# Kernel tuning notes

Measured on AMD Instinct MI355X. Metric: run time of the kernel, lower is better.

The kernel has to match this reference:

```python
import jax, jax.numpy as jnp
import numpy as np
import math

B, Q, CQ = 2, 2048, 512
H, D = 8, 64  # no_heads, c_hidden

def setup_inputs() -> dict:
    key = jax.random.key(0)
    ks = jax.random.split(key, 8)
    s = 0.02
    return {
        "q_x": jax.random.normal(ks[0], (B, Q, CQ), jnp.float32),
        "kv_x": jax.random.normal(ks[1], (B, Q, CQ), jnp.float32),
        "bias": jax.random.normal(ks[2], (B, 1, Q, Q), jnp.float32),
        "w_qkv": jax.random.normal(ks[3], (3 * H * D, CQ), jnp.float32) * s,
        "w_o": jax.random.normal(ks[4], (CQ, H * D), jnp.float32) * s,
        "b_o": jnp.zeros((CQ,), jnp.float32),
        "w_g": jax.random.normal(ks[5], (H * D, CQ), jnp.float32) * s,
        "b_g": jnp.zeros((H * D,), jnp.float32),
    }

def reference(q_x, kv_x, bias, w_qkv, w_o, b_o, w_g, b_g):
    # Fused QKV projection from q_x (kv_x is unused by the original module's _prep_qkv)
    qkv = jnp.einsum('bqc,ec->bqe', q_x, w_qkv)  # [B,Q,3*H*D]
    q, k, v = jnp.split(qkv, 3, axis=-1)
    q = q.reshape(B, Q, H, D) / math.sqrt(D)
    k = k.reshape(B, Q, H, D)
    v = v.reshape(B, Q, H, D)
    # scores + additive pairwise bias, softmax over keys
    scores = jnp.einsum('bqhd,bkhd->bhqk', q, k) + bias  # [B,H,Q,K]
    attn = jax.nn.softmax(scores, axis=-1)
    o = jnp.einsum('bhqk,bkhd->bqhd', attn, v)  # [B,Q,H,D]
    # sigmoid gating
    g = jax.nn.sigmoid(jnp.einsum('bqc,ec->bqe', q_x, w_g) + b_g).reshape(B, Q, H, D)
    o = o * g
    # output projection
    o = o.reshape(B, Q, H * D)
    return jnp.einsum('bqe,ce->bqc', o, w_o) + b_o
```

## Files before the change

kernel.cpp:

```cpp
#include <hip/hip_runtime.h>
#include <math.h>

#define B_  2
#define Q_  2048
#define CQ_ 512
#define H_  8
#define D_  64
#define M_  (B_*Q_)
#define L2E 1.44269504088896f

typedef __bf16 bf16;
typedef __bf16 bf16x4 __attribute__((ext_vector_type(4)));
typedef __bf16 bf16x8 __attribute__((ext_vector_type(8)));
typedef float  f32x4  __attribute__((ext_vector_type(4)));
typedef float  f32x16 __attribute__((ext_vector_type(16)));

__device__ __forceinline__ void gl_lds16(const bf16* g, bf16* l) {
    __builtin_amdgcn_global_load_lds(
        (const __attribute__((address_space(1))) unsigned int*)g,
        (__attribute__((address_space(3))) unsigned int*)l, 16, 0, 0);
}

__device__ __forceinline__ bf16x4 shfl_xor32(bf16x4 v) {
    union { bf16x4 h; int i[2]; } u;
    u.h = v;
    u.i[0] = __shfl_xor(u.i[0], 32, 64);
    u.i[1] = __shfl_xor(u.i[1], 32, 64);
    return u.h;
}

#define S0 (4096*512)
#define S1 (1536*512)
#define S2 (512*512)
#define S3 (512*512)
__global__ __launch_bounds__(256)
void convert_kernel(const float* __restrict__ qx, const float* __restrict__ wqkv,
                    const float* __restrict__ wg, const float* __restrict__ wo,
                    bf16* __restrict__ qxb, bf16* __restrict__ wcat, bf16* __restrict__ wob)
{
    const long long t = (long long)blockIdx.x * 256 + threadIdx.x;
    const long long e = t * 8;
    const float* src; bf16* dst;
    if (e < S0) {
        const int m = (int)(e >> 9), k = (int)(e & 511);
        src = qx + e;
        dst = qxb + (size_t)(k >> 5) * (4096 * 32) + (size_t)m * 32 + (k & 31);
    } else if (e < S0 + S1) {
        const long long e2 = e - S0;
        const int n = (int)(e2 >> 9), k = (int)(e2 & 511);
        src = wqkv + e2;
        dst = wcat + (size_t)(k >> 5) * (2048 * 32) + (size_t)n * 32 + (k & 31);
    } else if (e < S0 + S1 + S2) {
        const long long e2 = e - S0 - S1;
        const int n = 1536 + (int)(e2 >> 9), k = (int)(e2 & 511);
        src = wg + e2;
        dst = wcat + (size_t)(k >> 5) * (2048 * 32) + (size_t)n * 32 + (k & 31);
    } else {
        const long long e2 = e - S0 - S1 - S2;
        const int n = (int)(e2 >> 9), k = (int)(e2 & 511);
        src = wo + e2;
        dst = wob + (size_t)(k >> 5) * (512 * 32) + (size_t)n * 32 + (k & 31);
    }
    const float4 a = *(const float4*)(src);
    const float4 b = *(const float4*)(src + 4);
    bf16x8 v;
    v[0] = (bf16)a.x; v[1] = (bf16)a.y; v[2] = (bf16)a.z; v[3] = (bf16)a.w;
    v[4] = (bf16)b.x; v[5] = (bf16)b.y; v[6] = (bf16)b.z; v[7] = (bf16)b.w;
    *(bf16x8*)dst = v;
}

template<int BM, int BN, int EPI, int WNR, int APACK>
__global__ __launch_bounds__(256)
void gemm_bf16(const bf16* __restrict__ A, const bf16* __restrict__ W,
               const float* __restrict__ bvec, float* __restrict__ fout,
               bf16* __restrict__ qb, bf16* __restrict__ kb, bf16* __restrict__ vb,
               bf16* __restrict__ gb)
{
    constexpr int MI = BM / 32, NJ = BN / 32;
    constexpr int APARTS = BM / 16, BPARTS = BN / 16, NPARTS = APARTS + BPARTS;
    __shared__ __align__(16) bf16 As[2][BM * 32];
    __shared__ __align__(16) bf16 Bs[2][BN * 32];

    const int t = threadIdx.x;
    const int w = t >> 6, lane = t & 63;
    const int l15 = lane & 15, quad = lane >> 4;
    const int wm = w & 1, wn = w >> 1;
    const int bm = blockIdx.x * BM;
    const int bn = blockIdx.y * BN;
    const bool swapped = (EPI == 1) || ((bn >> 9) != 2);

    f32x4 acc[MI][NJ] = {};

    auto stage = [&](int kp, int buf) {
        #pragma unroll
        for (int idx = 0; idx < NPARTS / 4; ++idx) {
            const int p = idx * 4 + w;
            if (p < APARTS) {
                if constexpr (APACK)
                    gl_lds16(A + (size_t)kp * (4096 * 32) + (size_t)bm * 32 + p * 512 + lane * 8,
                             As[buf] + p * 512);
                else
                    gl_lds16(A + (size_t)(bm + p * 16 + (lane >> 2)) * 512 + kp * 32 + (lane & 3) * 8,
                             As[buf] + p * 512);
            } else {
                gl_lds16(W + (size_t)kp * (WNR * 32) + (size_t)bn * 32 + (p - APARTS) * 512 + lane * 8,
                         Bs[buf] + (p - APARTS) * 512);
            }
        }
    };

    stage(0, 0);
    __asm__ volatile("s_waitcnt vmcnt(0)" ::: "memory");
    __syncthreads();

    int cur = 0;
    #pragma unroll 1
    for (int kp = 0; kp < 16; ++kp) {
        if (kp < 15) stage(kp + 1, cur ^ 1);

        bf16x8 af[MI], bfr[NJ];
        #pragma unroll
        for (int i = 0; i < MI; ++i)
            af[i] = *(const bf16x8*)(As[cur] + (wm * (BM / 2) + i * 16 + l15) * 32 + quad * 8);
        #pragma unroll
        for (int j = 0; j < NJ; ++j)
            bfr[j] = *(const bf16x8*)(Bs[cur] + (wn * (BN / 2) + j * 16 + l15) * 32 + quad * 8);
        if (swapped) {
            #pragma unroll
            for (int i = 0; i < MI; ++i)
                #pragma unroll
                for (int j = 0; j < NJ; ++j)
                    acc[i][j] = __builtin_amdgcn_mfma_f32_16x16x32_bf16(bfr[j], af[i], acc[i][j], 0, 0, 0);
        } else {
            #pragma unroll
            for (int i = 0; i < MI; ++i)
                #pragma unroll
                for (int j = 0; j < NJ; ++j)
                    acc[i][j] = __builtin_amdgcn_mfma_f32_16x16x32_bf16(af[i], bfr[j], acc[i][j], 0, 0, 0);
        }
        __asm__ volatile("s_waitcnt vmcnt(0)" ::: "memory");
        __syncthreads();
        cur ^= 1;
    }

    if (swapped) {
        #pragma unroll
        for (int i = 0; i < MI; ++i) {
            const int m = bm + wm * (BM / 2) + i * 16 + l15;
            const int b = m >> 11, qq = m & 2047;
            #pragma unroll
            for (int j = 0; j < NJ; ++j) {
                const int n0 = bn + wn * (BN / 2) + j * 16 + quad * 4;
                const f32x4 cv = acc[i][j];
                if constexpr (EPI == 1) {
                    float4 st;
                    st.x = cv[0] + bvec[n0 + 0];
                    st.y = cv[1] + bvec[n0 + 1];
                    st.z = cv[2] + bvec[n0 + 2];
                    st.w = cv[3] + bvec[n0 + 3];
                    *(float4*)(fout + (size_t)m * 512 + n0) = st;
                } else {
                    const int part = n0 >> 9;
                    if (part == 0) {
                        const int h = (n0 >> 6) & 7, d0 = n0 & 63;
                        bf16x4 q4;
                        #pragma unroll
                        for (int r = 0; r < 4; ++r) q4[r] = (bf16)(cv[r] * (0.125f * L2E));
                        *(bf16x4*)(qb + (size_t)(b * H_ + h) * (Q_ * D_) + (size_t)qq * 64 + d0) = q4;
                    } else if (part == 1) {
                        const int h = (n0 >> 6) & 7, d0 = n0 & 63;
                        const size_t off = (size_t)(b * H_ + h) * (Q_ * D_)
                            + (qq >> 6) * 4096 + ((qq >> 5) & 1) * 2048
                            + (d0 >> 4) * 512 + ((d0 >> 3) & 1) * 256
                            + (qq & 31) * 8 + (d0 & 7);
                        bf16x4 k4;
                        #pragma unroll
                        for (int r = 0; r < 4; ++r) k4[r] = (bf16)cv[r];
                        *(bf16x4*)(kb + off) = k4;
                    } else {
                        const int gcol = n0 & 511;
                        const float4 bv4 = *(const float4*)(bvec + gcol);
                        bf16x4 g4;
                        g4[0] = (bf16)(1.f / (1.f + __expf(-(cv[0] + bv4.x))));
                        g4[1] = (bf16)(1.f / (1.f + __expf(-(cv[1] + bv4.y))));
                        g4[2] = (bf16)(1.f / (1.f + __expf(-(cv[2] + bv4.z))));
                        g4[3] = (bf16)(1.f / (1.f + __expf(-(cv[3] + bv4.w))));
                        *(bf16x4*)(gb + (size_t)m * 512 + gcol) = g4;
                    }
                }
            }
        }
    } else {
        #pragma unroll
        for (int i = 0; i < MI; ++i) {
            const int m0 = bm + wm * (BM / 2) + i * 16 + quad * 4;
            const int b = m0 >> 11, qq0 = m0 & 2047;
            #pragma unroll
            for (int j = 0; j < NJ; ++j) {
                const int n = bn + wn * (BN / 2) + j * 16 + l15;
                const int h = (n >> 6) & 7, d = n & 63;
                const size_t off = (size_t)(b * H_ + h) * (Q_ * D_)
                    + (qq0 >> 6) * 4096 + (d >> 5) * 2048
                    + ((qq0 & 63) >> 4) * 512 + ((qq0 >> 3) & 1) * 256
                    + (d & 31) * 8 + (qq0 & 7);
                bf16x4 v4;
                #pragma unroll
                for (int r = 0; r < 4; ++r) v4[r] = (bf16)acc[i][j][r];
                *(bf16x4*)(vb + off) = v4;
            }
        }
    }
}

__global__ __launch_bounds__(256, 3)
void attn_part(const bf16* __restrict__ qb, const bf16* __restrict__ kf,
               const bf16* __restrict__ vf, const float* __restrict__ bias,
               bf16* __restrict__ po, float* __restrict__ lsum)
{
    __shared__ __align__(16) bf16 Ks[2][4096];
    __shared__ __align__(16) bf16 Vs[2][4096];

    const int tid  = threadIdx.x;
    const int wv   = tid >> 6, lane = tid & 63;
    const int l31  = lane & 31, b5 = lane >> 5;
    const int x    = blockIdx.x;
    const int bh   = ((x & 7) << 1) | (x >> 3);
    const int b    = bh >> 3;
    const int qg   = blockIdx.y * 128 + wv * 32 + l31;
    const int ks   = blockIdx.z;
    const int start   = ks * 11;
    const int nsteps  = (ks == 2) ? 10 : 11;

    const bf16* qp = qb + ((size_t)bh * Q_ + qg) * D_;
    bf16x8 bq[4];
    #pragma unroll
    for (int c = 0; c < 4; ++c)
        bq[c] = *(const bf16x8*)(qp + c * 16 + b5 * 8);

    f32x16 acc[2] = {};
    float l_loc = 0.f;

    const bf16*  kfb  = kf + (size_t)bh * (Q_ * D_) + (size_t)start * 4096;
    const bf16*  vfb  = vf + (size_t)bh * (Q_ * D_) + (size_t)start * 4096;
    const float* brow = bias + ((size_t)b * Q_ + qg) * Q_ + start * 64;

    #pragma unroll
    for (int p = 0; p < 2; ++p) {
        gl_lds16(kfb + (wv * 2 + p) * 512 + lane * 8, Ks[0] + (wv * 2 + p) * 512);
        gl_lds16(vfb + (wv * 2 + p) * 512 + lane * 8, Vs[0] + (wv * 2 + p) * 512);
    }
    __asm__ volatile("s_waitcnt vmcnt(0)" ::: "memory");
    __syncthreads();

    int cur = 0;
    #pragma unroll 1
    for (int t = 0; t < nsteps; ++t) {
        if (t + 1 < nsteps) {
            const size_t off = (size_t)(t + 1) * 4096;
            #pragma unroll
            for (int p = 0; p < 2; ++p) {
                gl_lds16(kfb + off + (wv * 2 + p) * 512 + lane * 8,
                         Ks[cur ^ 1] + (wv * 2 + p) * 512);
                gl_lds16(vfb + off + (wv * 2 + p) * 512 + lane * 8,
                         Vs[cur ^ 1] + (wv * 2 + p) * 512);
            }
        }

        f32x4 bc[8];
        #pragma unroll
        for (int i = 0; i < 8; ++i)
            bc[i] = *(const f32x4*)(brow + t * 64 + (i >> 2) * 32 + (i & 3) * 8 + b5 * 4);

        const bf16* Kc = Ks[cur];
        f32x16 sv[2] = {};
        #pragma unroll
        for (int kg = 0; kg < 2; ++kg)
            #pragma unroll
            for (int c = 0; c < 4; ++c) {
                const bf16x8 ak = *(const bf16x8*)(Kc + kg * 2048 + c * 512 + lane * 8);
                sv[kg] = __builtin_amdgcn_mfma_f32_32x32x16_bf16(ak, bq[c], sv[kg], 0, 0, 0);
            }

        float sc[2][16];
        float rs = 0.f;
        #pragma unroll
        for (int kg = 0; kg < 2; ++kg)
            #pragma unroll
            for (int r = 0; r < 16; ++r) {
                sc[kg][r] = __builtin_amdgcn_exp2f(
                    fmaf(bc[kg * 4 + (r >> 2)][r & 3], L2E, sv[kg][r]));
                rs += sc[kg][r];
            }
        l_loc += rs;

        const bf16* Vc = Vs[cur];
        #pragma unroll
        for (int c4 = 0; c4 < 4; ++c4) {
            const int kg = c4 >> 1;
            const int base = (c4 & 1) * 8;
            bf16x4 g0, g1;
            #pragma unroll
            for (int r = 0; r < 4; ++r) {
                g0[r] = (bf16)sc[kg][base + r];
                g1[r] = (bf16)sc[kg][base + 4 + r];
            }
            const bf16x4 snd = b5 ? g0 : g1;
            const bf16x4 rcv = shfl_xor32(snd);
            const bf16x4 lo  = b5 ? rcv : g0;
            const bf16x4 hi  = b5 ? g1  : rcv;
            bf16x8 bp;
            #pragma unroll
            for (int r = 0; r < 4; ++r) { bp[r] = lo[r]; bp[4 + r] = hi[r]; }
            #pragma unroll
            for (int dg = 0; dg < 2; ++dg) {
                const bf16x8 av = *(const bf16x8*)(Vc + dg * 2048 + c4 * 512 + lane * 8);
                acc[dg] = __builtin_amdgcn_mfma_f32_32x32x16_bf16(av, bp, acc[dg], 0, 0, 0);
            }
        }

        __asm__ volatile("s_waitcnt vmcnt(0)" ::: "memory");
        __syncthreads();
        cur ^= 1;
    }

    const float l_run = l_loc + __shfl_xor(l_loc, 32, 64);
    const size_t pbase = ((size_t)(ks * 16 + bh) * Q_ + qg) * 64;
    #pragma unroll
    for (int dg = 0; dg < 2; ++dg)
        #pragma unroll
        for (int gi = 0; gi < 4; ++gi) {
            const int d0 = dg * 32 + gi * 8 + b5 * 4;
            bf16x4 ov;
            #pragma unroll
            for (int r = 0; r < 4; ++r)
                ov[r] = (bf16)acc[dg][gi * 4 + r];
            *(bf16x4*)(po + pbase + d0) = ov;
        }
    if (b5 == 0)
        lsum[(size_t)(ks * 16 + bh) * Q_ + qg] = l_run;
}

__global__ __launch_bounds__(256)
void merge_kernel(const bf16* __restrict__ po, const float* __restrict__ lsum,
                  const bf16* g, bf16* og)
{
    const int gid = blockIdx.x * 256 + threadIdx.x;
    const int row = gid >> 3;
    const int d8  = (gid & 7) * 8;
    const int bh  = row >> 11, qg = row & 2047;
    const int b   = bh >> 3, h = bh & 7;

    const float inv = 1.f / (lsum[row] + lsum[16 * Q_ + row] + lsum[32 * Q_ + row]);

    const bf16x8 o0 = *(const bf16x8*)(po + (size_t)row * 64 + d8);
    const bf16x8 o1 = *(const bf16x8*)(po + (size_t)16 * Q_ * 64 + (size_t)row * 64 + d8);
    const bf16x8 o2 = *(const bf16x8*)(po + (size_t)32 * Q_ * 64 + (size_t)row * 64 + d8);
    const size_t obase = ((size_t)(b * Q_ + qg)) * 512 + h * 64 + d8;
    const bf16x8 gv = *(const bf16x8*)(g + obase);
    bf16x8 ov;
    #pragma unroll
    for (int r = 0; r < 8; ++r)
        ov[r] = (bf16)(((float)o0[r] + (float)o1[r] + (float)o2[r]) * inv * (float)gv[r]);
    *(bf16x8*)(og + obase) = ov;
}

extern "C" void kernel_launch(void* const* d_in, const int* in_sizes, int n_in,
                              void* d_out, int out_size, void* d_ws, size_t ws_size,
                              hipStream_t stream)
{
    const float* q_x   = (const float*)d_in[0];
    const float* bias  = (const float*)d_in[2];
    const float* w_qkv = (const float*)d_in[3];
    const float* w_o   = (const float*)d_in[4];
    const float* b_o   = (const float*)d_in[5];
    const float* w_g   = (const float*)d_in[6];
    const float* b_g   = (const float*)d_in[7];
    float* out = (float*)d_out;

    char* ws = (char*)d_ws;
    bf16*  po   = (bf16*)(ws);
    bf16*  qxb  = (bf16*)(ws);
    bf16*  wcat = (bf16*)(ws + (4u  << 20));
    bf16*  qb   = (bf16*)(ws + (12u << 20));
    bf16*  kb   = (bf16*)(ws + (16u << 20));
    bf16*  vb   = (bf16*)(ws + (20u << 20));
    bf16*  gb   = (bf16*)(ws + (24u << 20));
    bf16*  wob  = (bf16*)(ws + (28u << 20));
    float* lsum = (float*)(ws + (28u << 20) + (1u << 19));

    convert_kernel<<<(S0 + S1 + S2 + S3) / (256 * 8), 256, 0, stream>>>(
        q_x, w_qkv, w_g, w_o, qxb, wcat, wob);
    gemm_bf16<128, 64, 0, 2048, 1><<<dim3(32, 32), 256, 0, stream>>>(
        qxb, wcat, b_g, nullptr, qb, kb, vb, gb);
    attn_part<<<dim3(B_ * H_, Q_ / 128, 3), 256, 0, stream>>>(qb, kb, vb, bias, po, lsum);
    merge_kernel<<<(16 * Q_ * 8) / 256, 256, 0, stream>>>(po, lsum, gb, gb);
    gemm_bf16<64, 64, 1, 512, 0><<<dim3(64, 8), 256, 0, stream>>>(
        gb, wob, b_o, out, nullptr, nullptr, nullptr, nullptr);
}
```

Baseline: 187.3 us.

## Triple-buffer GEMM and attention, pre-convert bias to bf16, widen QKV GEMM tile

Moves the GEMM and attention main loops from double to triple buffering in LDS. Each iteration now waits with a partial vmcnt count and a barrier instead of a full drain at the end. A new pass converts the pairwise bias to bf16, pre-scaled by log2(e), so attention reads half the bias bytes and can fold the bias into the score initialisation; this pass runs only when the workspace is large enough. The QKV GEMM tile is widened to 128x128. The changes trade extra LDS per block (lower occupancy), an extra full pass over the bias, and lower bias precision for less memory traffic and more load/compute overlap.

```diff
diff --git a/kernel.cpp b/kernel.cpp
--- a/kernel.cpp
+++ b/kernel.cpp
@@ -69,6 +69,20 @@
     *(bf16x8*)dst = v;
 }
 
+__global__ __launch_bounds__(256)
+void convert_bias(const float* __restrict__ bias, bf16* __restrict__ biasb)
+{
+    const size_t e = ((size_t)blockIdx.x * 256 + threadIdx.x) * 8;
+    const float4 a = *(const float4*)(bias + e);
+    const float4 b = *(const float4*)(bias + e + 4);
+    bf16x8 v;
+    v[0] = (bf16)(a.x * L2E); v[1] = (bf16)(a.y * L2E);
+    v[2] = (bf16)(a.z * L2E); v[3] = (bf16)(a.w * L2E);
+    v[4] = (bf16)(b.x * L2E); v[5] = (bf16)(b.y * L2E);
+    v[6] = (bf16)(b.z * L2E); v[7] = (bf16)(b.w * L2E);
+    *(bf16x8*)(biasb + e) = v;
+}
+
 template<int BM, int BN, int EPI, int WNR, int APACK>
 __global__ __launch_bounds__(256)
 void gemm_bf16(const bf16* __restrict__ A, const bf16* __restrict__ W,
@@ -78,8 +92,9 @@
 {
     constexpr int MI = BM / 32, NJ = BN / 32;
     constexpr int APARTS = BM / 16, BPARTS = BN / 16, NPARTS = APARTS + BPARTS;
-    __shared__ __align__(16) bf16 As[2][BM * 32];
-    __shared__ __align__(16) bf16 Bs[2][BN * 32];
+    constexpr int G = NPARTS / 4;
+    __shared__ __align__(16) bf16 As[3][BM * 32];
+    __shared__ __align__(16) bf16 Bs[3][BN * 32];
 
     const int t = threadIdx.x;
     const int w = t >> 6, lane = t & 63;
@@ -91,40 +106,45 @@
 
     f32x4 acc[MI][NJ] = {};
 
-    auto stage = [&](int kp, int buf) {
-        #pragma unroll
-        for (int idx = 0; idx < NPARTS / 4; ++idx) {
+    auto stage = [&](int kp) {
+        bf16* Ad = As[kp % 3];
+        bf16* Bd = Bs[kp % 3];
+        #pragma unroll
+        for (int idx = 0; idx < G; ++idx) {
             const int p = idx * 4 + w;
             if (p < APARTS) {
                 if constexpr (APACK)
                     gl_lds16(A + (size_t)kp * (4096 * 32) + (size_t)bm * 32 + p * 512 + lane * 8,
-                             As[buf] + p * 512);
+                             Ad + p * 512);
                 else
                     gl_lds16(A + (size_t)(bm + p * 16 + (lane >> 2)) * 512 + kp * 32 + (lane & 3) * 8,
-                             As[buf] + p * 512);
+                             Ad + p * 512);
             } else {
                 gl_lds16(W + (size_t)kp * (WNR * 32) + (size_t)bn * 32 + (p - APARTS) * 512 + lane * 8,
-                         Bs[buf] + (p - APARTS) * 512);
+                         Bd + (p - APARTS) * 512);
             }
         }
     };
 
-    stage(0, 0);
-    __asm__ volatile("s_waitcnt vmcnt(0)" ::: "memory");
-    __syncthreads();
-
-    int cur = 0;
+    stage(0);
+    stage(1);
+
     #pragma unroll 1
     for (int kp = 0; kp < 16; ++kp) {
-        if (kp < 15) stage(kp + 1, cur ^ 1);
-
+        if (kp == 15) __builtin_amdgcn_s_waitcnt(0x0F70);
+        else          __builtin_amdgcn_s_waitcnt(0x0F70 | G);
+        __builtin_amdgcn_s_barrier();
+        __asm__ volatile("" ::: "memory");
+
+        const bf16* Ac = As[kp % 3];
+        const bf16* Bc = Bs[kp % 3];
         bf16x8 af[MI], bfr[NJ];
         #pragma unroll
         for (int i = 0; i < MI; ++i)
-            af[i] = *(const bf16x8*)(As[cur] + (wm * (BM / 2) + i * 16 + l15) * 32 + quad * 8);
+            af[i] = *(const bf16x8*)(Ac + (wm * (BM / 2) + i * 16 + l15) * 32 + quad * 8);
         #pragma unroll
         for (int j = 0; j < NJ; ++j)
-            bfr[j] = *(const bf16x8*)(Bs[cur] + (wn * (BN / 2) + j * 16 + l15) * 32 + quad * 8);
+            bfr[j] = *(const bf16x8*)(Bc + (wn * (BN / 2) + j * 16 + l15) * 32 + quad * 8);
         if (swapped) {
             #pragma unroll
             for (int i = 0; i < MI; ++i)
@@ -138,9 +158,8 @@
                 for (int j = 0; j < NJ; ++j)
                     acc[i][j] = __builtin_amdgcn_mfma_f32_16x16x32_bf16(af[i], bfr[j], acc[i][j], 0, 0, 0);
         }
-        __asm__ volatile("s_waitcnt vmcnt(0)" ::: "memory");
-        __syncthreads();
-        cur ^= 1;
+
+        if (kp + 2 < 16) stage(kp + 2);
     }
 
     if (swapped) {
@@ -212,13 +231,14 @@
     }
 }
 
+template<int BB>
 __global__ __launch_bounds__(256, 3)
 void attn_part(const bf16* __restrict__ qb, const bf16* __restrict__ kf,
-               const bf16* __restrict__ vf, const float* __restrict__ bias,
+               const bf16* __restrict__ vf, const void* __restrict__ biasp,
                bf16* __restrict__ po, float* __restrict__ lsum)
 {
-    __shared__ __align__(16) bf16 Ks[2][4096];
-    __shared__ __align__(16) bf16 Vs[2][4096];
+    __shared__ __align__(16) bf16 Ks[3][4096];
+    __shared__ __align__(16) bf16 Vs[3][4096];
 
     const int tid  = threadIdx.x;
     const int wv   = tid >> 6, lane = tid & 63;
@@ -228,8 +248,8 @@
     const int b    = bh >> 3;
     const int qg   = blockIdx.y * 128 + wv * 32 + l31;
     const int ks   = blockIdx.z;
-    const int start   = ks * 11;
-    const int nsteps  = (ks == 2) ? 10 : 11;
+    const int start  = ks * 11;
+    const int nsteps = (ks == 2) ? 10 : 11;
 
     const bf16* qp = qb + ((size_t)bh * Q_ + qg) * D_;
     bf16x8 bq[4];
@@ -240,39 +260,52 @@
     f32x16 acc[2] = {};
     float l_loc = 0.f;
 
-    const bf16*  kfb  = kf + (size_t)bh * (Q_ * D_) + (size_t)start * 4096;
-    const bf16*  vfb  = vf + (size_t)bh * (Q_ * D_) + (size_t)start * 4096;
-    const float* brow = bias + ((size_t)b * Q_ + qg) * Q_ + start * 64;
-
-    #pragma unroll
-    for (int p = 0; p < 2; ++p) {
-        gl_lds16(kfb + (wv * 2 + p) * 512 + lane * 8, Ks[0] + (wv * 2 + p) * 512);
-        gl_lds16(vfb + (wv * 2 + p) * 512 + lane * 8, Vs[0] + (wv * 2 + p) * 512);
-    }
-    __asm__ volatile("s_waitcnt vmcnt(0)" ::: "memory");
-    __syncthreads();
-
-    int cur = 0;
+    const bf16*  kfb   = kf + (size_t)bh * (Q_ * D_) + (size_t)start * 4096;
+    const bf16*  vfb   = vf + (size_t)bh * (Q_ * D_) + (size_t)start * 4096;
+    const bf16*  browh = (const bf16*)biasp  + ((size_t)b * Q_ + qg) * Q_ + start * 64;
+    const float* browf = (const float*)biasp + ((size_t)b * Q_ + qg) * Q_ + start * 64;
+
+    auto stageKV = [&](int tt) {
+        const size_t off = (size_t)tt * 4096;
+        bf16* Kd = Ks[tt % 3];
+        bf16* Vd = Vs[tt % 3];
+        #pragma unroll
+        for (int p = 0; p < 2; ++p) {
+            gl_lds16(kfb + off + (wv * 2 + p) * 512 + lane * 8, Kd + (wv * 2 + p) * 512);
+            gl_lds16(vfb + off + (wv * 2 + p) * 512 + lane * 8, Vd + (wv * 2 + p) * 512);
+        }
+    };
+
+    bf16x4 bbh[8];
+    f32x4  bbf[8];
+    auto loadBias = [&](int tt) {
+        #pragma unroll
+        for (int i = 0; i < 8; ++i) {
+            const int o = tt * 64 + (i >> 2) * 32 + (i & 3) * 8 + b5 * 4;
+            if constexpr (BB) bbh[i] = *(const bf16x4*)(browh + o);
+            else              bbf[i] = *(const f32x4*)(browf + o);
+        }
+    };
+
+    stageKV(0);
+    stageKV(1);
+    loadBias(0);
+
     #pragma unroll 1
     for (int t = 0; t < nsteps; ++t) {
-        if (t + 1 < nsteps) {
-            const size_t off = (size_t)(t + 1) * 4096;
-            #pragma unroll
-            for (int p = 0; p < 2; ++p) {
-                gl_lds16(kfb + off + (wv * 2 + p) * 512 + lane * 8,
-                         Ks[cur ^ 1] + (wv * 2 + p) * 512);
-                gl_lds16(vfb + off + (wv * 2 + p) * 512 + lane * 8,
-                         Vs[cur ^ 1] + (wv * 2 + p) * 512);
-            }
-        }
-
-        f32x4 bc[8];
-        #pragma unroll
-        for (int i = 0; i < 8; ++i)
-            bc[i] = *(const f32x4*)(brow + t * 64 + (i >> 2) * 32 + (i & 3) * 8 + b5 * 4);
-
-        const bf16* Kc = Ks[cur];
-        f32x16 sv[2] = {};
+        if (t == nsteps - 1) __builtin_amdgcn_s_waitcnt(0x0F78);
+        else                 __builtin_amdgcn_s_waitcnt(0x0F7C);
+        __builtin_amdgcn_s_barrier();
+        __asm__ volatile("" ::: "memory");
+
+        const bf16* Kc = Ks[t % 3];
+        f32x16 sv[2];
+        #pragma unroll
+        for (int kg = 0; kg < 2; ++kg)
+            #pragma unroll
+            for (int r = 0; r < 16; ++r)
+                sv[kg][r] = BB ? (float)bbh[kg * 4 + (r >> 2)][r & 3]
+                               : bbf[kg * 4 + (r >> 2)][r & 3] * L2E;
         #pragma unroll
         for (int kg = 0; kg < 2; ++kg)
             #pragma unroll
@@ -287,13 +320,12 @@
         for (int kg = 0; kg < 2; ++kg)
             #pragma unroll
             for (int r = 0; r < 16; ++r) {
-                sc[kg][r] = __builtin_amdgcn_exp2f(
-                    fmaf(bc[kg * 4 + (r >> 2)][r & 3], L2E, sv[kg][r]));
+                sc[kg][r] = __builtin_amdgcn_exp2f(sv[kg][r]);
                 rs += sc[kg][r];
             }
         l_loc += rs;
 
-        const bf16* Vc = Vs[cur];
+        const bf16* Vc = Vs[t % 3];
         #pragma unroll
         for (int c4 = 0; c4 < 4; ++c4) {
             const int kg = c4 >> 1;
@@ -318,9 +350,8 @@
             }
         }
 
-        __asm__ volatile("s_waitcnt vmcnt(0)" ::: "memory");
-        __syncthreads();
-        cur ^= 1;
+        if (t + 1 < nsteps) loadBias(t + 1);
+        if (t + 2 < nsteps) stageKV(t + 2);
     }
 
     const float l_run = l_loc + __shfl_xor(l_loc, 32, 64);
@@ -378,21 +409,31 @@
     float* out = (float*)d_out;
 
     char* ws = (char*)d_ws;
-    bf16*  po   = (bf16*)(ws);
-    bf16*  qxb  = (bf16*)(ws);
-    bf16*  wcat = (bf16*)(ws + (4u  << 20));
-    bf16*  qb   = (bf16*)(ws + (12u << 20));
-    bf16*  kb   = (bf16*)(ws + (16u << 20));
-    bf16*  vb   = (bf16*)(ws + (20u << 20));
-    bf16*  gb   = (bf16*)(ws + (24u << 20));
-    bf16*  wob  = (bf16*)(ws + (28u << 20));
-    float* lsum = (float*)(ws + (28u << 20) + (1u << 19));
+    bf16*  po    = (bf16*)(ws);
+    bf16*  qxb   = (bf16*)(ws);
+    bf16*  wcat  = (bf16*)(ws + (4u  << 20));
+    bf16*  qb    = (bf16*)(ws + (12u << 20));
+    bf16*  kb    = (bf16*)(ws + (16u << 20));
+    bf16*  vb    = (bf16*)(ws + (20u << 20));
+    bf16*  gb    = (bf16*)(ws + (24u << 20));
+    bf16*  wob   = (bf16*)(ws + (28u << 20));
+    float* lsum  = (float*)(ws + (28u << 20) + (1u << 19));
+    bf16*  biasb = (bf16*)(ws + (29u << 20));
+
+    const bool use_bb = ws_size >= (46ull << 20);
 
     convert_kernel<<<(S0 + S1 + S2 + S3) / (256 * 8), 256, 0, stream>>>(
         q_x, w_qkv, w_g, w_o, qxb, wcat, wob);
-    gemm_bf16<128, 64, 0, 2048, 1><<<dim3(32, 32), 256, 0, stream>>>(
+    if (use_bb)
+        convert_bias<<<(2 * Q_ * Q_) / (256 * 8), 256, 0, stream>>>(bias, biasb);
+    gemm_bf16<128, 128, 0, 2048, 1><<<dim3(32, 16), 256, 0, stream>>>(
         qxb, wcat, b_g, nullptr, qb, kb, vb, gb);
-    attn_part<<<dim3(B_ * H_, Q_ / 128, 3), 256, 0, stream>>>(qb, kb, vb, bias, po, lsum);
+    if (use_bb)
+        attn_part<1><<<dim3(B_ * H_, Q_ / 128, 3), 256, 0, stream>>>(
+            qb, kb, vb, biasb, po, lsum);
+    else
+        attn_part<0><<<dim3(B_ * H_, Q_ / 128, 3), 256, 0, stream>>>(
+            qb, kb, vb, bias, po, lsum);
     merge_kernel<<<(16 * Q_ * 8) / 256, 256, 0, stream>>>(po, lsum, gb, gb);
     gemm_bf16<64, 64, 1, 512, 0><<<dim3(64, 8), 256, 0, stream>>>(
         gb, wob, b_o, out, nullptr, nullptr, nullptr, nullptr);
```

New measurement: 180.3 us. 1.04x faster.
